# Optimization experiments

Hardware: AMD Instinct MI355X
Metric: run time of the kernel (lower is better)

## Reference

```python
import jax, jax.numpy as jnp
import numpy as np

D = 2048  # d_model
B = 64    # batch
S = 32    # seq_len (module is designed for 32-step sequences)
C = 8     # number of control embeddings
INITRANGE = 0.1


def setup_inputs() -> dict:
    key = jax.random.key(0)
    ks = jax.random.split(key, 6)

    def lin_w(k):
        return jax.random.uniform(k, (D, D), minval=-INITRANGE, maxval=INITRANGE, dtype=jnp.float32)

    zb = jnp.zeros((D,), dtype=jnp.float32)
    return {
        "sequence": jax.random.normal(ks[0], (B, S, D), dtype=jnp.float32),
        "controls": jax.random.normal(ks[1], (C, B, D), dtype=jnp.float32),
        "Wq": lin_w(ks[2]), "bq": zb,
        "Wk": lin_w(ks[3]), "bk": zb,
        "Wv": lin_w(ks[4]), "bv": zb,
        "Wo": lin_w(ks[5]), "bo": zb,
    }


def reference(sequence, controls, Wq, bq, Wk, bk, Wv, bv, Wo, bo):
    # sequence: (B, S, D); controls: (C, B, D) = stacked list of control embeddings.
    d = sequence.shape[-1]
    queries = sequence @ Wq.T + bq            # (B, S, D)
    keys = controls @ Wk.T + bk               # (C, B, D)  == control_key(c).unsqueeze(1)
    values = controls @ Wv.T + bv             # (C, B, D)
    # bmm(queries, keys^T) with a single key per control -> scores (C, B, S, 1)
    scores = jnp.einsum('bsd,cbd->cbs', queries, keys)[..., None] / jnp.sqrt(jnp.asarray(d, sequence.dtype))
    attn = jax.nn.softmax(scores, axis=-1)    # softmax over a size-1 axis -> exactly 1.0
    attended = attn * values[:, :, None, :]   # (C, B, S, D); bmm(attn, values)
    # dropout is identity in eval mode
    projected = jnp.einsum('cbsd,ed->cbse', attended, Wo) + bo  # per-control output_proj
    # residual accumulation over the control loop == sum over C
    return sequence + projected.sum(axis=0)
```

## Files before the change

### kernel.cpp

```cpp
#include <hip/hip_runtime.h>
#include <hip/hip_bf16.h>

#define DM 2048
#define BB 64
#define SS 32
#define CC 8

typedef __attribute__((ext_vector_type(8))) short short8;
typedef __attribute__((ext_vector_type(4))) short short4v;
typedef __attribute__((ext_vector_type(4))) float f32x4;

static __device__ __forceinline__ short f2bf(float f) {
  union { __hip_bfloat16 h; short s; } u;
  u.h = __float2bfloat16(f);
  return u.s;
}

__global__ void k1_sum_bf16(const float* __restrict__ controls,
                            short* __restrict__ u16) {
  const int idx = blockIdx.x * 128 + threadIdx.x;
  const int b = idx >> 9;
  const int k = (idx & 511) * 4;
  float4 s = make_float4(0.f, 0.f, 0.f, 0.f);
#pragma unroll
  for (int c = 0; c < CC; ++c) {
    const float4 v = *reinterpret_cast<const float4*>(
        controls + ((size_t)c * BB + b) * DM + k);
    s.x += v.x; s.y += v.y; s.z += v.z; s.w += v.w;
  }
  short4v o = {f2bf(s.x), f2bf(s.y), f2bf(s.z), f2bf(s.w)};
  *reinterpret_cast<short4v*>(u16 + (size_t)b * DM + k) = o;
}

template <int EPI>
__global__ __launch_bounds__(256, 2) void gemm_full(
    const short* __restrict__ abf, const float* __restrict__ w,
    const float* __restrict__ bias, short* __restrict__ vout,
    const float* __restrict__ seq, float* __restrict__ out) {
  __shared__ float lwW[4][2][16 * 128];
  __shared__ f32x4 red[3][64];
  __shared__ float ptt[16][16];

  const int t    = threadIdx.x;
  const int lane = t & 63;
  const int wv   = t >> 6;
  const int eb   = blockIdx.x & 127;
  const int bg   = blockIdx.x >> 7;
  const int e0   = eb * 16;
  const int b0   = bg * 16;
  const int kq   = wv * 512;

  const int wrl = lane >> 5, wg = lane & 31;
  const int r = lane & 15, ksub = lane >> 4;
  const int q = r & 7;

  const short* abase = abf + (size_t)(b0 + r) * DM + kq + ksub * 8;

  short8 areg[2][4];
  f32x4 acc = {0.f, 0.f, 0.f, 0.f};

  {
    float* wd = &lwW[wv][0][0];
#pragma unroll
    for (int i = 0; i < 8; ++i) {
      const int row = 2 * i + wrl;
      const float* src =
          w + (size_t)(e0 + row) * DM + kq + ((wg ^ (row & 7)) << 2);
      __builtin_amdgcn_global_load_lds(
          (const __attribute__((address_space(1))) void*)src,
          (__attribute__((address_space(3))) void*)(wd + i * 256), 16, 0, 0);
    }
#pragma unroll
    for (int s = 0; s < 4; ++s)
      areg[0][s] = *reinterpret_cast<const short8*>(abase + s * 32);
  }

#pragma unroll
  for (int c = 0; c < 4; ++c) {
    if (c < 3) {
      const int ck = (c + 1) * 128;
      float* wd = &lwW[wv][(c + 1) & 1][0];
#pragma unroll
      for (int i = 0; i < 8; ++i) {
        const int row = 2 * i + wrl;
        const float* src =
            w + (size_t)(e0 + row) * DM + kq + ck + ((wg ^ (row & 7)) << 2);
        __builtin_amdgcn_global_load_lds(
            (const __attribute__((address_space(1))) void*)src,
            (__attribute__((address_space(3))) void*)(wd + i * 256), 16, 0, 0);
      }
#pragma unroll
      for (int s = 0; s < 4; ++s)
        areg[(c + 1) & 1][s] =
            *reinterpret_cast<const short8*>(abase + ck + s * 32);
      asm volatile("s_waitcnt vmcnt(12)" ::: "memory");
    } else {
      asm volatile("s_waitcnt vmcnt(0)" ::: "memory");
    }
    __builtin_amdgcn_sched_barrier(0);

    const float* wb = &lwW[wv][c & 1][0];
#pragma unroll
    for (int s = 0; s < 4; ++s) {
      const int glW = s * 8 + ksub * 2;
      const float4 lo = *reinterpret_cast<const float4*>(
          wb + r * 128 + ((glW ^ q) << 2));
      const float4 hi = *reinterpret_cast<const float4*>(
          wb + r * 128 + (((glW + 1) ^ q) << 2));
      short8 bf;
      bf[0] = f2bf(lo.x); bf[1] = f2bf(lo.y);
      bf[2] = f2bf(lo.z); bf[3] = f2bf(lo.w);
      bf[4] = f2bf(hi.x); bf[5] = f2bf(hi.y);
      bf[6] = f2bf(hi.z); bf[7] = f2bf(hi.w);
      acc = __builtin_amdgcn_mfma_f32_16x16x32_bf16(areg[c & 1][s], bf, acc,
                                                    0, 0, 0);
    }
  }

  if (wv != 0) red[wv - 1][lane] = acc;
  __syncthreads();
  if (wv == 0) {
    acc += red[0][lane];
    acc += red[1][lane];
    acc += red[2][lane];
    const float be = 8.f * bias[e0 + r];
    if (EPI == 0) {
#pragma unroll
      for (int j = 0; j < 4; ++j)
        vout[(size_t)(b0 + ksub * 4 + j) * DM + e0 + r] = f2bf(acc[j] + be);
    } else {
#pragma unroll
      for (int j = 0; j < 4; ++j) ptt[ksub * 4 + j][r] = acc[j] + be;
    }
  }

  if (EPI == 1) {
    __syncthreads();
    const int ef = (t & 3) * 4;
    const int sl = (t >> 2) & 3;
    const int bl = t >> 4;
    const float4 pv = *reinterpret_cast<const float4*>(&ptt[bl][ef]);
#pragma unroll
    for (int i = 0; i < 8; ++i) {
      const int s = sl + i * 4;
      const size_t off = ((size_t)(b0 + bl) * SS + s) * DM + e0 + ef;
      const float4 qd = *reinterpret_cast<const float4*>(seq + off);
      *reinterpret_cast<float4*>(out + off) =
          make_float4(qd.x + pv.x, qd.y + pv.y, qd.z + pv.z, qd.w + pv.w);
    }
  }
}

extern "C" void kernel_launch(void* const* d_in, const int* in_sizes, int n_in,
                              void* d_out, int out_size, void* d_ws,
                              size_t ws_size, hipStream_t stream) {
  const float* seq      = (const float*)d_in[0];
  const float* controls = (const float*)d_in[1];
  const float* Wv = (const float*)d_in[6];
  const float* bv = (const float*)d_in[7];
  const float* Wo = (const float*)d_in[8];
  const float* bo = (const float*)d_in[9];
  float* out = (float*)d_out;

  char* ws = (char*)d_ws;
  short* u16 = (short*)(ws);
  short* v16 = (short*)(ws + (512ull << 10));

  k1_sum_bf16<<<256, 128, 0, stream>>>(controls, u16);
  gemm_full<0><<<512, 256, 0, stream>>>(u16, Wv, bv, v16, nullptr, nullptr);
  gemm_full<1><<<512, 256, 0, stream>>>(v16, Wo, bo, nullptr, seq, out);
}
```

Baseline: 32.47 us.

## Split GEMM K dimension across eight waves instead of four per block

Doubles the block size to 512 threads so each wave handles a 256-wide K slice instead of 512. Each pipelined chunk shrinks to 64 columns, and the LDS swizzle, wait counts, cross-wave reduction and epilogue store mapping are adjusted to match. The aim is more in-flight memory parallelism and latency hiding per CU for these small, memory-bound GEMMs. The cost is a larger cross-wave reduction and more wave overhead per block.

Result: slower. 34.08 us (+4.9%).

```diff
diff --git a/kernel.cpp b/kernel.cpp
--- a/kernel.cpp
+++ b/kernel.cpp
@@ -33,12 +33,12 @@
 }
 
 template <int EPI>
-__global__ __launch_bounds__(256, 2) void gemm_full(
+__global__ __launch_bounds__(512, 4) void gemm_full(
     const short* __restrict__ abf, const float* __restrict__ w,
     const float* __restrict__ bias, short* __restrict__ vout,
     const float* __restrict__ seq, float* __restrict__ out) {
-  __shared__ float lwW[4][2][16 * 128];
-  __shared__ f32x4 red[3][64];
+  __shared__ float lwW[8][2][16 * 64];
+  __shared__ f32x4 red[7][64];
   __shared__ float ptt[16][16];
 
   const int t    = threadIdx.x;
@@ -48,52 +48,45 @@
   const int bg   = blockIdx.x >> 7;
   const int e0   = eb * 16;
   const int b0   = bg * 16;
-  const int kq   = wv * 512;
+  const int kq   = wv * 256;
 
-  const int wrl = lane >> 5, wg = lane & 31;
+  const int srow4 = lane >> 4;
+  const int sg    = lane & 15;
   const int r = lane & 15, ksub = lane >> 4;
-  const int q = r & 7;
 
   const short* abase = abf + (size_t)(b0 + r) * DM + kq + ksub * 8;
 
-  short8 areg[2][4];
+  short8 areg[2][2];
   f32x4 acc = {0.f, 0.f, 0.f, 0.f};
 
-  {
-    float* wd = &lwW[wv][0][0];
-#pragma unroll
-    for (int i = 0; i < 8; ++i) {
-      const int row = 2 * i + wrl;
-      const float* src =
-          w + (size_t)(e0 + row) * DM + kq + ((wg ^ (row & 7)) << 2);
-      __builtin_amdgcn_global_load_lds(
-          (const __attribute__((address_space(1))) void*)src,
-          (__attribute__((address_space(3))) void*)(wd + i * 256), 16, 0, 0);
-    }
-#pragma unroll
-    for (int s = 0; s < 4; ++s)
-      areg[0][s] = *reinterpret_cast<const short8*>(abase + s * 32);
+#define ISSUE_W(c, bsel)                                                      \
+  {                                                                           \
+    const int ck = kq + (c) * 64;                                             \
+    float* wd = &lwW[wv][bsel][0];                                            \
+    _Pragma("unroll") for (int i = 0; i < 4; ++i) {                           \
+      const int row = 4 * i + srow4;                                          \
+      const float* src =                                                      \
+          w + (size_t)(e0 + row) * DM + ck + ((sg ^ row) << 2);               \
+      __builtin_amdgcn_global_load_lds(                                       \
+          (const __attribute__((address_space(1))) void*)src,                 \
+          (__attribute__((address_space(3))) void*)(wd + i * 256), 16, 0, 0); \
+    }                                                                         \
   }
+#define LOAD_A(c, bsel)                                                       \
+  {                                                                           \
+    areg[bsel][0] = *reinterpret_cast<const short8*>(abase + (c) * 64);       \
+    areg[bsel][1] = *reinterpret_cast<const short8*>(abase + (c) * 64 + 32);  \
+  }
+
+  ISSUE_W(0, 0)
+  LOAD_A(0, 0)
 
 #pragma unroll
   for (int c = 0; c < 4; ++c) {
     if (c < 3) {
-      const int ck = (c + 1) * 128;
-      float* wd = &lwW[wv][(c + 1) & 1][0];
-#pragma unroll
-      for (int i = 0; i < 8; ++i) {
-        const int row = 2 * i + wrl;
-        const float* src =
-            w + (size_t)(e0 + row) * DM + kq + ck + ((wg ^ (row & 7)) << 2);
-        __builtin_amdgcn_global_load_lds(
-            (const __attribute__((address_space(1))) void*)src,
-            (__attribute__((address_space(3))) void*)(wd + i * 256), 16, 0, 0);
-      }
-#pragma unroll
-      for (int s = 0; s < 4; ++s)
-        areg[(c + 1) & 1][s] =
-            *reinterpret_cast<const short8*>(abase + ck + s * 32);
-      asm volatile("s_waitcnt vmcnt(12)" ::: "memory");
+      ISSUE_W(c + 1, (c + 1) & 1)
+      LOAD_A(c + 1, (c + 1) & 1)
+      asm volatile("s_waitcnt vmcnt(6)" ::: "memory");
     } else {
       asm volatile("s_waitcnt vmcnt(0)" ::: "memory");
     }
@@ -101,12 +94,12 @@
 
     const float* wb = &lwW[wv][c & 1][0];
 #pragma unroll
-    for (int s = 0; s < 4; ++s) {
-      const int glW = s * 8 + ksub * 2;
-      const float4 lo = *reinterpret_cast<const float4*>(
-          wb + r * 128 + ((glW ^ q) << 2));
+    for (int s = 0; s < 2; ++s) {
+      const int gl = s * 8 + ksub * 2;
+      const float4 lo =
+          *reinterpret_cast<const float4*>(wb + r * 64 + ((gl ^ r) << 2));
       const float4 hi = *reinterpret_cast<const float4*>(
-          wb + r * 128 + (((glW + 1) ^ q) << 2));
+          wb + r * 64 + (((gl + 1) ^ r) << 2));
       short8 bf;
       bf[0] = f2bf(lo.x); bf[1] = f2bf(lo.y);
       bf[2] = f2bf(lo.z); bf[3] = f2bf(lo.w);
@@ -116,13 +109,14 @@
                                                     0, 0, 0);
     }
   }
+#undef ISSUE_W
+#undef LOAD_A
 
   if (wv != 0) red[wv - 1][lane] = acc;
   __syncthreads();
   if (wv == 0) {
-    acc += red[0][lane];
-    acc += red[1][lane];
-    acc += red[2][lane];
+#pragma unroll
+    for (int i = 0; i < 7; ++i) acc += red[i][lane];
     const float be = 8.f * bias[e0 + r];
     if (EPI == 0) {
 #pragma unroll
@@ -137,12 +131,12 @@
   if (EPI == 1) {
     __syncthreads();
     const int ef = (t & 3) * 4;
-    const int sl = (t >> 2) & 3;
-    const int bl = t >> 4;
+    const int sl = (t >> 2) & 7;
+    const int bl = t >> 5;
     const float4 pv = *reinterpret_cast<const float4*>(&ptt[bl][ef]);
 #pragma unroll
-    for (int i = 0; i < 8; ++i) {
-      const int s = sl + i * 4;
+    for (int i = 0; i < 4; ++i) {
+      const int s = sl + i * 8;
       const size_t off = ((size_t)(b0 + bl) * SS + s) * DM + e0 + ef;
       const float4 qd = *reinterpret_cast<const float4*>(seq + off);
       *reinterpret_cast<float4*>(out + off) =
@@ -167,6 +161,6 @@
   short* v16 = (short*)(ws + (512ull << 10));
 
   k1_sum_bf16<<<256, 128, 0, stream>>>(controls, u16);
-  gemm_full<0><<<512, 256, 0, stream>>>(u16, Wv, bv, v16, nullptr, nullptr);
-  gemm_full<1><<<512, 256, 0, stream>>>(v16, Wo, bo, nullptr, seq, out);
+  gemm_full<0><<<512, 512, 0, stream>>>(u16, Wv, bv, v16, nullptr, nullptr);
+  gemm_full<1><<<512, 512, 0, stream>>>(v16, Wo, bo, nullptr, seq, out);
 }
```
